# Optimization experiments

Hardware: AMD Instinct MI355X
Metric: run time of the kernel (lower is better)

The kernel has to match this reference:

```python
import jax, jax.numpy as jnp
import numpy as np

EMBEDDING_SIZE = 50
MAX_DOCUMENT_LENGTH = 100
MAX_LABEL = 15
VOCAB = 200000
HID = 1024
BATCH = 4096


def setup_inputs() -> dict:
    key = jax.random.key(0)
    ks = jax.random.split(key, 8)
    x = jax.random.randint(ks[0], (BATCH, MAX_DOCUMENT_LENGTH), 0, VOCAB)
    emb_table = jax.random.normal(ks[1], (VOCAB, EMBEDDING_SIZE), jnp.float32) * 0.05
    # Keras GRUCell (reset_after=True): kernel [E,3H], recurrent_kernel [H,3H],
    # bias [2,3H] split into input bias and recurrent bias; gate order z, r, h.
    kernel = jax.random.normal(ks[2], (EMBEDDING_SIZE, 3 * HID), jnp.float32) * (1.0 / np.sqrt(EMBEDDING_SIZE))
    rec_kernel = jax.random.normal(ks[3], (HID, 3 * HID), jnp.float32) * (1.0 / np.sqrt(HID))
    bias_i = jnp.zeros((3 * HID,), jnp.float32)
    bias_r = jnp.zeros((3 * HID,), jnp.float32)
    Wd = jax.random.normal(ks[4], (HID, MAX_LABEL), jnp.float32) * (1.0 / np.sqrt(HID))
    bd = jnp.zeros((MAX_LABEL,), jnp.float32)
    return {"x": x, "drop_rate": 0, "emb_table": emb_table, "kernel": kernel,
            "rec_kernel": rec_kernel, "bias_i": bias_i, "bias_r": bias_r,
            "Wd": Wd, "bd": bd}


def _gru_scan(emb, kernel, rec_kernel, bias_i, bias_r):
    # emb: [B,T,E] -> time-major [T,B,E]
    emb_t = jnp.transpose(emb, (1, 0, 2))
    B = emb.shape[0]
    h0 = jnp.zeros((B, HID), emb.dtype)

    def step(h, x_t):
        xp = x_t @ kernel + bias_i            # [B,3H]
        hp = h @ rec_kernel + bias_r          # [B,3H]
        xz, xr, xh = jnp.split(xp, 3, axis=-1)
        hz, hr, hh = jnp.split(hp, 3, axis=-1)
        z = jax.nn.sigmoid(xz + hz)
        r = jax.nn.sigmoid(xr + hr)
        hcand = jnp.tanh(xh + r * hh)
        h_new = z * h + (1.0 - z) * hcand
        return h_new, None

    h_last, _ = jax.lax.scan(step, h0, emb_t)
    return h_last


def reference(x, drop_rate, emb_table, kernel, rec_kernel, bias_i, bias_r, Wd, bd):
    emb = emb_table[x]                         # [B,T,E]
    encoding = _gru_scan(emb, kernel, rec_kernel, bias_i, bias_r)  # [B,H]
    if drop_rate > 0:                          # drop_rate is a static Python int
        keep = 1.0 - float(drop_rate)
        mask = jax.random.bernoulli(jax.random.key(1), keep, encoding.shape)
        encoding = jnp.where(mask, encoding / keep, 0.0)
    logits = encoding @ Wd + bd                # [B,15]
    return logits
```

## Files before the change

### kernel.cpp

```cpp
#include <hip/hip_runtime.h>
#include <stdint.h>

#define H_DIM   1024
#define G3      3072
#define EMB     50
#define TSTEPS  100
#define NB      4096
#define NLABEL  15

typedef __bf16 bf16x8 __attribute__((ext_vector_type(8)));
typedef float  f32x4  __attribute__((ext_vector_type(4)));

__device__ inline uint16_t f2bf(float f) {
  uint32_t u = __builtin_bit_cast(uint32_t, f);
  u += 0x7FFFu + ((u >> 16) & 1u);
  return (uint16_t)(u >> 16);
}

__device__ inline void gld16(const void* g, void* l) {
  __builtin_amdgcn_global_load_lds(
      (const __attribute__((address_space(1))) uint32_t*)g,
      (__attribute__((address_space(3))) uint32_t*)l, 16, 0, 0);
}

#define BARF() do { __builtin_amdgcn_s_barrier(); \
                    asm volatile("" ::: "memory"); } while (0)


__global__ __launch_bounds__(256) void prep_recT(const float* __restrict__ rec,
                                                 uint16_t* __restrict__ recT) {
  __shared__ uint16_t st[64][72];
  const int n0 = blockIdx.x * 64;
  const int k0 = blockIdx.y * 64;
  const int tid = threadIdx.x;
#pragma unroll
  for (int i = 0; i < 16; ++i) {
    int idx = tid + i * 256;
    int r = idx >> 6;
    int c = idx & 63;
    st[c][r] = f2bf(rec[(size_t)(k0 + r) * G3 + n0 + c]);
  }
  __syncthreads();
#pragma unroll
  for (int i = 0; i < 16; ++i) {
    int idx = tid + i * 256;
    int r = idx >> 6;
    int c = idx & 63;
    recT[(size_t)(n0 + r) * H_DIM + k0 + c] = st[r][c];
  }
}

__global__ __launch_bounds__(256) void prep_kerT(const float* __restrict__ ker,
                                                 uint16_t* __restrict__ kerT) {
  int n = blockIdx.x * 4 + (threadIdx.x >> 6);
  int k = threadIdx.x & 63;
  float v = (k < EMB) ? ker[(size_t)k * G3 + n] : 0.f;
  kerT[(size_t)n * 64 + k] = f2bf(v);
}

__global__ __launch_bounds__(256) void prep_embt(const int* __restrict__ x,
                                                 const float* __restrict__ tab,
                                                 uint16_t* __restrict__ embt) {
  int idx = blockIdx.x * 256 + threadIdx.x;
  int g = idx >> 5;
  int p = idx & 31;
  int t = g >> 12;
  int b = g & 4095;
  int row = x[b * TSTEPS + t];
  float2 v;
  if (p < 25) v = *reinterpret_cast<const float2*>(tab + (size_t)row * EMB + 2 * p);
  else { v.x = 0.f; v.y = 0.f; }
  uint32_t packed = (uint32_t)f2bf(v.x) | ((uint32_t)f2bf(v.y) << 16);
  *reinterpret_cast<uint32_t*>(embt + (size_t)g * 64 + 2 * p) = packed;
}

__global__ __launch_bounds__(512, 2) void gru_step_kernel(
    const uint16_t* __restrict__ hb_prev,
    float* __restrict__ hf,
    uint16_t* __restrict__ hb_next,
    const uint16_t* __restrict__ recT,
    const uint16_t* __restrict__ kerT,
    const uint16_t* __restrict__ embt,
    const float* __restrict__ bias_i,
    const float* __restrict__ bias_r) {
  __shared__ __align__(16) uint16_t sA2[2][128 * 64];
  __shared__ __align__(16) uint16_t sP[2][3][128 * 64];

  const int tid  = threadIdx.x;
  const int lane = tid & 63;
  const int wid  = tid >> 6;
  const int wm   = wid >> 2;
  const int wn   = wid & 3;
  const int bid  = blockIdx.x;
  const int xk = bid & 7, slot = bid >> 3;
  const int rowblk = (xk >> 1) * 8 + (slot >> 2);
  const int colblk = (xk & 1) * 4 + (slot & 3);
  const int r0 = rowblk * 128;
  const int j0 = colblk * 128;

  const int swz8 = 8 * ((lane & 7) ^ (lane >> 3));

  bf16x8 af[4][2];
  bf16x8 bf0[2][2], bf1[2][2];
  f32x4 accZ[4][2], accR[4][2], accH[4][2], accX[4][2];
#pragma unroll
  for (int m = 0; m < 4; ++m)
#pragma unroll
    for (int n = 0; n < 2; ++n) {
      accZ[m][n] = (f32x4){0.f, 0.f, 0.f, 0.f};
      accR[m][n] = (f32x4){0.f, 0.f, 0.f, 0.f};
      accH[m][n] = (f32x4){0.f, 0.f, 0.f, 0.f};
      accX[m][n] = (f32x4){0.f, 0.f, 0.f, 0.f};
    }

  auto stageA = [&](int t) {
    const int abuf = t & 1;
#pragma unroll
    for (int i = 0; i < 2; ++i) {
      int row = wid * 16 + i * 8 + (lane >> 3);
      const uint16_t* src = (t < 16)
          ? hb_prev + (size_t)(r0 + row) * H_DIM + t * 64 + swz8
          : embt + (size_t)(r0 + row) * 64 + swz8;
      gld16(src, &sA2[abuf][(wid * 128 + i * 64 + lane) * 8]);
    }
  };
  auto stageP = [&](int t, int g) {
    const int pbuf = t & 1;
#pragma unroll
    for (int i = 0; i < 2; ++i) {
      int c = wid * 2 + i;
      int n = c * 8 + (lane >> 3);
      const uint16_t* src = (t < 16)
          ? recT + ((size_t)g * H_DIM + j0 + n) * H_DIM + t * 64 + swz8
          : kerT + ((size_t)g * H_DIM + j0 + n) * 64 + swz8;
      gld16(src, &sP[pbuf][g][(c * 64 + lane) * 8]);
    }
  };
  auto readA = [&](int t) {
    const int abuf = t & 1;
#pragma unroll
    for (int ks = 0; ks < 2; ++ks) {
      const int colswz = (ks * 32 + (lane >> 4) * 8) ^ ((lane & 7) << 3);
#pragma unroll
      for (int mf = 0; mf < 4; ++mf)
        af[mf][ks] = *reinterpret_cast<const bf16x8*>(
            &sA2[abuf][(wm * 64 + mf * 16 + (lane & 15)) * 64 + colswz]);
    }
  };
  auto readB = [&](int t, int g, bf16x8 (&bf)[2][2]) {
    const int pbuf = t & 1;
#pragma unroll
    for (int ks = 0; ks < 2; ++ks) {
      const int colswz = (ks * 32 + (lane >> 4) * 8) ^ ((lane & 7) << 3);
#pragma unroll
      for (int nf = 0; nf < 2; ++nf) {
        int nn = wn * 32 + nf * 16 + (lane & 15);
        bf[nf][ks] = *reinterpret_cast<const bf16x8*>(&sP[pbuf][g][nn * 64 + colswz]);
      }
    }
  };
  auto MF = [&](bf16x8 (&bf)[2][2], f32x4 (&acc)[4][2]) {
    __builtin_amdgcn_s_setprio(1);
#pragma unroll
    for (int ks = 0; ks < 2; ++ks)
#pragma unroll
      for (int nf = 0; nf < 2; ++nf)
#pragma unroll
        for (int mf = 0; mf < 4; ++mf)
          acc[mf][nf] = __builtin_amdgcn_mfma_f32_16x16x32_bf16(
              af[mf][ks], bf[nf][ks], acc[mf][nf], 0, 0, 0);
    __builtin_amdgcn_s_setprio(0);
  };

#define PH(DSRD, MFBUF, MFACC, STG, WN) do { \
    DSRD; MF(MFBUF, MFACC); STG; \
    asm volatile("s_waitcnt vmcnt(" #WN ")" ::: "memory"); \
    BARF(); \
  } while (0)
#define PHH(MFBUF, MFACC, DSRD, STG, WN) do { \
    MF(MFBUF, MFACC); DSRD; STG; \
    asm volatile("s_waitcnt vmcnt(" #WN ")" ::: "memory"); \
    BARF(); \
  } while (0)
#define TILE_STEADY(t, BFA, BFB) do { \
    PH(readB(t, 1, BFB), BFA, accZ, stageP((t) + 1, 1), 6); \
    PH(readB(t, 2, BFA), BFB, accR, stageP((t) + 1, 2), 4); \
    PHH(BFA, accH, (readA((t) + 1), readB((t) + 1, 0, BFB)), \
        (stageA((t) + 2), stageP((t) + 2, 0)), 6); \
  } while (0)

  stageA(0); stageP(0, 0); stageP(0, 1); stageP(0, 2);
  stageA(1); stageP(1, 0);
  asm volatile("s_waitcnt vmcnt(0)" ::: "memory");
  BARF();
  readA(0); readB(0, 0, bf0);

  for (int tt = 0; tt < 14; tt += 2) {
    TILE_STEADY(tt, bf0, bf1);
    TILE_STEADY(tt + 1, bf1, bf0);
  }
  TILE_STEADY(14, bf0, bf1);
  PH(readB(15, 1, bf0), bf1, accZ, stageP(16, 1), 6);
  PH(readB(15, 2, bf1), bf0, accR, stageP(16, 2), 4);
  PHH(bf1, accH, (readA(16), readB(16, 0, bf0)), (void)0, 2);
  PH(readB(16, 1, bf1), bf0, accZ, (void)0, 0);
  PH(readB(16, 2, bf0), bf1, accR, (void)0, 0);
  MF(bf0, accX);

#pragma unroll
  for (int nf = 0; nf < 2; ++nf) {
    int col = j0 + wn * 32 + nf * 16 + (lane & 15);
    float b_z = bias_i[col] + bias_r[col];
    float b_r = bias_i[H_DIM + col] + bias_r[H_DIM + col];
    float bih = bias_i[2 * H_DIM + col];
    float brh = bias_r[2 * H_DIM + col];
#pragma unroll
    for (int mf = 0; mf < 4; ++mf) {
#pragma unroll
      for (int q = 0; q < 4; ++q) {
        int row = r0 + wm * 64 + mf * 16 + (lane >> 4) * 4 + q;
        float z  = 1.f / (1.f + __expf(-(accZ[mf][nf][q] + b_z)));
        float rr = 1.f / (1.f + __expf(-(accR[mf][nf][q] + b_r)));
        float pre = accX[mf][nf][q] + bih + rr * (accH[mf][nf][q] + brh);
        float hc  = 2.f / (1.f + __expf(-2.f * pre)) - 1.f;
        size_t idx = (size_t)row * H_DIM + col;
        float hold = hf[idx];
        float hnew = z * hold + (1.f - z) * hc;
        hf[idx] = hnew;
        hb_next[idx] = f2bf(hnew);
      }
    }
  }
#undef PH
#undef PHH
#undef TILE_STEADY
}

__global__ __launch_bounds__(64) void logits_kernel(const float* __restrict__ hf,
                                                    const float* __restrict__ Wd,
                                                    const float* __restrict__ bd,
                                                    float* __restrict__ out) {
  int b = blockIdx.x;
  int l = threadIdx.x;
  float p[NLABEL];
#pragma unroll
  for (int o = 0; o < NLABEL; ++o) p[o] = 0.f;
  for (int kb = 0; kb < 16; ++kb) {
    int k = kb * 64 + l;
    float hv = hf[(size_t)b * H_DIM + k];
#pragma unroll
    for (int o = 0; o < NLABEL; ++o) p[o] += hv * Wd[k * NLABEL + o];
  }
#pragma unroll
  for (int o = 0; o < NLABEL; ++o) {
#pragma unroll
    for (int s = 32; s; s >>= 1) p[o] += __shfl_xor(p[o], s);
  }
  if (l == 0) {
#pragma unroll
    for (int o = 0; o < NLABEL; ++o) out[(size_t)b * NLABEL + o] = p[o] + bd[o];
  }
}

extern "C" void kernel_launch(void* const* d_in, const int* in_sizes, int n_in,
                              void* d_out, int out_size, void* d_ws, size_t ws_size,
                              hipStream_t stream) {
  const int*   x          = (const int*)d_in[0];
  const float* emb_table  = (const float*)d_in[2];
  const float* kernel_w   = (const float*)d_in[3];
  const float* rec_kernel = (const float*)d_in[4];
  const float* bias_i     = (const float*)d_in[5];
  const float* bias_r     = (const float*)d_in[6];
  const float* Wd         = (const float*)d_in[7];
  const float* bd         = (const float*)d_in[8];
  float* out = (float*)d_out;

  char* ws = (char*)d_ws;
  size_t off = 0;
  auto alloc = [&](size_t bytes) {
    char* p = ws + off;
    off += (bytes + 255) & ~(size_t)255;
    return p;
  };
  float*    hf   = (float*)alloc((size_t)NB * H_DIM * 4);
  uint16_t* hb0  = (uint16_t*)alloc((size_t)NB * H_DIM * 2);
  uint16_t* hb1  = (uint16_t*)alloc((size_t)NB * H_DIM * 2);
  uint16_t* recT = (uint16_t*)alloc((size_t)G3 * H_DIM * 2);
  uint16_t* kerT = (uint16_t*)alloc((size_t)G3 * 64 * 2);
  uint16_t* embt = (uint16_t*)alloc((size_t)TSTEPS * NB * 64 * 2);
  if (off > ws_size) return;

  hipMemsetAsync(hf, 0, (size_t)NB * H_DIM * 4, stream);
  hipMemsetAsync(hb0, 0, (size_t)NB * H_DIM * 2, stream);

  prep_recT<<<dim3(G3 / 64, H_DIM / 64), 256, 0, stream>>>(rec_kernel, recT);
  prep_kerT<<<G3 / 4, 256, 0, stream>>>(kernel_w, kerT);
  prep_embt<<<TSTEPS * NB * 32 / 256, 256, 0, stream>>>(x, emb_table, embt);

  uint16_t* hb[2] = {hb0, hb1};
  for (int t = 0; t < TSTEPS; ++t) {
    gru_step_kernel<<<256, 512, 0, stream>>>(
        hb[t & 1], hf, hb[(t + 1) & 1], recT, kerT,
        embt + (size_t)t * NB * 64, bias_i, bias_r);
  }
  logits_kernel<<<NB, 64, 0, stream>>>(hf, Wd, bd, out);
}
```

Before: 3.458 ms.

## Fuse GRU timesteps into one persistent cooperative kernel with per-rowblock barriers

Replaces the 100 per-timestep kernel launches with a single cooperative persistent kernel that loops over timesteps. The fp32 hidden state stays in registers instead of being read and written in global memory each step, and hf is written only at the final step. Blocks sharing a row block synchronise through an atomic counter. This is meant to remove launch gaps and global h traffic. It relies on all 256 blocks being co-resident and adds spin-wait barrier overhead.

```diff
diff --git a/kernel.cpp b/kernel.cpp
--- a/kernel.cpp
+++ b/kernel.cpp
@@ -74,15 +74,16 @@
   *reinterpret_cast<uint32_t*>(embt + (size_t)g * 64 + 2 * p) = packed;
 }
 
-__global__ __launch_bounds__(512, 2) void gru_step_kernel(
-    const uint16_t* __restrict__ hb_prev,
+__global__ __launch_bounds__(512, 2) void gru_persistent(
+    uint16_t* __restrict__ hb0,
+    uint16_t* __restrict__ hb1,
     float* __restrict__ hf,
-    uint16_t* __restrict__ hb_next,
     const uint16_t* __restrict__ recT,
     const uint16_t* __restrict__ kerT,
-    const uint16_t* __restrict__ embt,
+    const uint16_t* __restrict__ embt_all,
     const float* __restrict__ bias_i,
-    const float* __restrict__ bias_r) {
+    const float* __restrict__ bias_r,
+    uint32_t* __restrict__ cnt) {
   __shared__ __align__(16) uint16_t sA2[2][128 * 64];
   __shared__ __align__(16) uint16_t sP[2][3][128 * 64];
 
@@ -100,77 +101,99 @@
 
   const int swz8 = 8 * ((lane & 7) ^ (lane >> 3));
 
+  float c_bz[2], c_br[2], c_bih[2], c_brh[2];
+#pragma unroll
+  for (int nf = 0; nf < 2; ++nf) {
+    int col = j0 + wn * 32 + nf * 16 + (lane & 15);
+    c_bz[nf]  = bias_i[col] + bias_r[col];
+    c_br[nf]  = bias_i[H_DIM + col] + bias_r[H_DIM + col];
+    c_bih[nf] = bias_i[2 * H_DIM + col];
+    c_brh[nf] = bias_r[2 * H_DIM + col];
+  }
+
+  f32x4 hreg[4][2];
+#pragma unroll
+  for (int m = 0; m < 4; ++m)
+#pragma unroll
+    for (int n = 0; n < 2; ++n) hreg[m][n] = (f32x4){0.f, 0.f, 0.f, 0.f};
+
   bf16x8 af[4][2];
   bf16x8 bf0[2][2], bf1[2][2];
   f32x4 accZ[4][2], accR[4][2], accH[4][2], accX[4][2];
-#pragma unroll
-  for (int m = 0; m < 4; ++m)
-#pragma unroll
-    for (int n = 0; n < 2; ++n) {
-      accZ[m][n] = (f32x4){0.f, 0.f, 0.f, 0.f};
-      accR[m][n] = (f32x4){0.f, 0.f, 0.f, 0.f};
-      accH[m][n] = (f32x4){0.f, 0.f, 0.f, 0.f};
-      accX[m][n] = (f32x4){0.f, 0.f, 0.f, 0.f};
-    }
-
-  auto stageA = [&](int t) {
-    const int abuf = t & 1;
-#pragma unroll
-    for (int i = 0; i < 2; ++i) {
-      int row = wid * 16 + i * 8 + (lane >> 3);
-      const uint16_t* src = (t < 16)
-          ? hb_prev + (size_t)(r0 + row) * H_DIM + t * 64 + swz8
-          : embt + (size_t)(r0 + row) * 64 + swz8;
-      gld16(src, &sA2[abuf][(wid * 128 + i * 64 + lane) * 8]);
-    }
-  };
-  auto stageP = [&](int t, int g) {
-    const int pbuf = t & 1;
-#pragma unroll
-    for (int i = 0; i < 2; ++i) {
-      int c = wid * 2 + i;
-      int n = c * 8 + (lane >> 3);
-      const uint16_t* src = (t < 16)
-          ? recT + ((size_t)g * H_DIM + j0 + n) * H_DIM + t * 64 + swz8
-          : kerT + ((size_t)g * H_DIM + j0 + n) * 64 + swz8;
-      gld16(src, &sP[pbuf][g][(c * 64 + lane) * 8]);
-    }
-  };
-  auto readA = [&](int t) {
-    const int abuf = t & 1;
-#pragma unroll
-    for (int ks = 0; ks < 2; ++ks) {
-      const int colswz = (ks * 32 + (lane >> 4) * 8) ^ ((lane & 7) << 3);
-#pragma unroll
-      for (int mf = 0; mf < 4; ++mf)
-        af[mf][ks] = *reinterpret_cast<const bf16x8*>(
-            &sA2[abuf][(wm * 64 + mf * 16 + (lane & 15)) * 64 + colswz]);
-    }
-  };
-  auto readB = [&](int t, int g, bf16x8 (&bf)[2][2]) {
-    const int pbuf = t & 1;
-#pragma unroll
-    for (int ks = 0; ks < 2; ++ks) {
-      const int colswz = (ks * 32 + (lane >> 4) * 8) ^ ((lane & 7) << 3);
-#pragma unroll
-      for (int nf = 0; nf < 2; ++nf) {
-        int nn = wn * 32 + nf * 16 + (lane & 15);
-        bf[nf][ks] = *reinterpret_cast<const bf16x8*>(&sP[pbuf][g][nn * 64 + colswz]);
-      }
-    }
-  };
-  auto MF = [&](bf16x8 (&bf)[2][2], f32x4 (&acc)[4][2]) {
-    __builtin_amdgcn_s_setprio(1);
-#pragma unroll
-    for (int ks = 0; ks < 2; ++ks)
-#pragma unroll
-      for (int nf = 0; nf < 2; ++nf)
+
+  for (int s = 0; s < TSTEPS; ++s) {
+    const uint16_t* __restrict__ hb_prev = (s & 1) ? hb1 : hb0;
+    uint16_t* __restrict__ hb_next       = (s & 1) ? hb0 : hb1;
+    const uint16_t* __restrict__ emb = embt_all + (size_t)s * NB * 64;
+
+#pragma unroll
+    for (int m = 0; m < 4; ++m)
+#pragma unroll
+      for (int n = 0; n < 2; ++n) {
+        accZ[m][n] = (f32x4){0.f, 0.f, 0.f, 0.f};
+        accR[m][n] = (f32x4){0.f, 0.f, 0.f, 0.f};
+        accH[m][n] = (f32x4){0.f, 0.f, 0.f, 0.f};
+        accX[m][n] = (f32x4){0.f, 0.f, 0.f, 0.f};
+      }
+
+    auto stageA = [&](int t) {
+      const int abuf = t & 1;
+#pragma unroll
+      for (int i = 0; i < 2; ++i) {
+        int row = wid * 16 + i * 8 + (lane >> 3);
+        const uint16_t* src = (t < 16)
+            ? hb_prev + (size_t)(r0 + row) * H_DIM + t * 64 + swz8
+            : emb + (size_t)(r0 + row) * 64 + swz8;
+        gld16(src, &sA2[abuf][(wid * 128 + i * 64 + lane) * 8]);
+      }
+    };
+    auto stageP = [&](int t, int g) {
+      const int pbuf = t & 1;
+#pragma unroll
+      for (int i = 0; i < 2; ++i) {
+        int c = wid * 2 + i;
+        int n = c * 8 + (lane >> 3);
+        const uint16_t* src = (t < 16)
+            ? recT + ((size_t)g * H_DIM + j0 + n) * H_DIM + t * 64 + swz8
+            : kerT + ((size_t)g * H_DIM + j0 + n) * 64 + swz8;
+        gld16(src, &sP[pbuf][g][(c * 64 + lane) * 8]);
+      }
+    };
+    auto readA = [&](int t) {
+      const int abuf = t & 1;
+#pragma unroll
+      for (int ks = 0; ks < 2; ++ks) {
+        const int colswz = (ks * 32 + (lane >> 4) * 8) ^ ((lane & 7) << 3);
 #pragma unroll
         for (int mf = 0; mf < 4; ++mf)
-          acc[mf][nf] = __builtin_amdgcn_mfma_f32_16x16x32_bf16(
-              af[mf][ks], bf[nf][ks], acc[mf][nf], 0, 0, 0);
-    __builtin_amdgcn_s_setprio(0);
-  };
+          af[mf][ks] = *reinterpret_cast<const bf16x8*>(
+              &sA2[abuf][(wm * 64 + mf * 16 + (lane & 15)) * 64 + colswz]);
+      }
+    };
+    auto readB = [&](int t, int g, bf16x8 (&bf)[2][2]) {
+      const int pbuf = t & 1;
+#pragma unroll
+      for (int ks = 0; ks < 2; ++ks) {
+        const int colswz = (ks * 32 + (lane >> 4) * 8) ^ ((lane & 7) << 3);
+#pragma unroll
+        for (int nf = 0; nf < 2; ++nf) {
+          int nn = wn * 32 + nf * 16 + (lane & 15);
+          bf[nf][ks] = *reinterpret_cast<const bf16x8*>(&sP[pbuf][g][nn * 64 + colswz]);
+        }
+      }
+    };
+    auto MF = [&](bf16x8 (&bf)[2][2], f32x4 (&acc)[4][2]) {
+      __builtin_amdgcn_s_setprio(1);
+#pragma unroll
+      for (int ks = 0; ks < 2; ++ks)
+#pragma unroll
+        for (int nf = 0; nf < 2; ++nf)
+#pragma unroll
+          for (int mf = 0; mf < 4; ++mf)
+            acc[mf][nf] = __builtin_amdgcn_mfma_f32_16x16x32_bf16(
+                af[mf][ks], bf[nf][ks], acc[mf][nf], 0, 0, 0);
+      __builtin_amdgcn_s_setprio(0);
+    };
 
 #define PH(DSRD, MFBUF, MFACC, STG, WN) do { \
     DSRD; MF(MFBUF, MFACC); STG; \
@@ -189,51 +212,62 @@
         (stageA((t) + 2), stageP((t) + 2, 0)), 6); \
   } while (0)
 
-  stageA(0); stageP(0, 0); stageP(0, 1); stageP(0, 2);
-  stageA(1); stageP(1, 0);
-  asm volatile("s_waitcnt vmcnt(0)" ::: "memory");
-  BARF();
-  readA(0); readB(0, 0, bf0);
-
-  for (int tt = 0; tt < 14; tt += 2) {
-    TILE_STEADY(tt, bf0, bf1);
-    TILE_STEADY(tt + 1, bf1, bf0);
-  }
-  TILE_STEADY(14, bf0, bf1);
-  PH(readB(15, 1, bf0), bf1, accZ, stageP(16, 1), 6);
-  PH(readB(15, 2, bf1), bf0, accR, stageP(16, 2), 4);
-  PHH(bf1, accH, (readA(16), readB(16, 0, bf0)), (void)0, 2);
-  PH(readB(16, 1, bf1), bf0, accZ, (void)0, 0);
-  PH(readB(16, 2, bf0), bf1, accR, (void)0, 0);
-  MF(bf0, accX);
-
-#pragma unroll
-  for (int nf = 0; nf < 2; ++nf) {
-    int col = j0 + wn * 32 + nf * 16 + (lane & 15);
-    float b_z = bias_i[col] + bias_r[col];
-    float b_r = bias_i[H_DIM + col] + bias_r[H_DIM + col];
-    float bih = bias_i[2 * H_DIM + col];
-    float brh = bias_r[2 * H_DIM + col];
-#pragma unroll
-    for (int mf = 0; mf < 4; ++mf) {
-#pragma unroll
-      for (int q = 0; q < 4; ++q) {
-        int row = r0 + wm * 64 + mf * 16 + (lane >> 4) * 4 + q;
-        float z  = 1.f / (1.f + __expf(-(accZ[mf][nf][q] + b_z)));
-        float rr = 1.f / (1.f + __expf(-(accR[mf][nf][q] + b_r)));
-        float pre = accX[mf][nf][q] + bih + rr * (accH[mf][nf][q] + brh);
-        float hc  = 2.f / (1.f + __expf(-2.f * pre)) - 1.f;
-        size_t idx = (size_t)row * H_DIM + col;
-        float hold = hf[idx];
-        float hnew = z * hold + (1.f - z) * hc;
-        hf[idx] = hnew;
-        hb_next[idx] = f2bf(hnew);
-      }
+    stageA(0); stageP(0, 0); stageP(0, 1); stageP(0, 2);
+    stageA(1); stageP(1, 0);
+    asm volatile("s_waitcnt vmcnt(0)" ::: "memory");
+    BARF();
+    readA(0); readB(0, 0, bf0);
+
+    for (int tt = 0; tt < 14; tt += 2) {
+      TILE_STEADY(tt, bf0, bf1);
+      TILE_STEADY(tt + 1, bf1, bf0);
     }
-  }
+    TILE_STEADY(14, bf0, bf1);
+    PH(readB(15, 1, bf0), bf1, accZ, stageP(16, 1), 6);
+    PH(readB(15, 2, bf1), bf0, accR, stageP(16, 2), 4);
+    PHH(bf1, accH, (readA(16), readB(16, 0, bf0)), (void)0, 2);
+    PH(readB(16, 1, bf1), bf0, accZ, (void)0, 0);
+    PH(readB(16, 2, bf0), bf1, accR, (void)0, 0);
+    MF(bf0, accX);
+
 #undef PH
 #undef PHH
 #undef TILE_STEADY
+
+#pragma unroll
+    for (int nf = 0; nf < 2; ++nf) {
+      int col = j0 + wn * 32 + nf * 16 + (lane & 15);
+#pragma unroll
+      for (int mf = 0; mf < 4; ++mf) {
+#pragma unroll
+        for (int q = 0; q < 4; ++q) {
+          int row = r0 + wm * 64 + mf * 16 + (lane >> 4) * 4 + q;
+          float z  = 1.f / (1.f + __expf(-(accZ[mf][nf][q] + c_bz[nf])));
+          float rr = 1.f / (1.f + __expf(-(accR[mf][nf][q] + c_br[nf])));
+          float pre = accX[mf][nf][q] + c_bih[nf] +
+                      rr * (accH[mf][nf][q] + c_brh[nf]);
+          float hc  = 2.f / (1.f + __expf(-2.f * pre)) - 1.f;
+          float hnew = z * hreg[mf][nf][q] + (1.f - z) * hc;
+          hreg[mf][nf][q] = hnew;
+          size_t idx = (size_t)row * H_DIM + col;
+          hb_next[idx] = f2bf(hnew);
+          if (s == TSTEPS - 1) hf[idx] = hnew;
+        }
+      }
+    }
+
+    __syncthreads();
+    if (tid == 0) {
+      __threadfence();
+      __hip_atomic_fetch_add(&cnt[rowblk], 1u, __ATOMIC_RELEASE,
+                             __HIP_MEMORY_SCOPE_AGENT);
+      const uint32_t target = 8u * (uint32_t)(s + 1);
+      while (__hip_atomic_load(&cnt[rowblk], __ATOMIC_ACQUIRE,
+                               __HIP_MEMORY_SCOPE_AGENT) < target)
+        __builtin_amdgcn_s_sleep(2);
+    }
+    __syncthreads();
+  }
 }
 
 __global__ __launch_bounds__(64) void logits_kernel(const float* __restrict__ hf,
@@ -288,20 +322,24 @@
   uint16_t* recT = (uint16_t*)alloc((size_t)G3 * H_DIM * 2);
   uint16_t* kerT = (uint16_t*)alloc((size_t)G3 * 64 * 2);
   uint16_t* embt = (uint16_t*)alloc((size_t)TSTEPS * NB * 64 * 2);
+  uint32_t* cnt  = (uint32_t*)alloc(256);
   if (off > ws_size) return;
 
-  hipMemsetAsync(hf, 0, (size_t)NB * H_DIM * 4, stream);
   hipMemsetAsync(hb0, 0, (size_t)NB * H_DIM * 2, stream);
+  hipMemsetAsync(cnt, 0, 256, stream);
 
   prep_recT<<<dim3(G3 / 64, H_DIM / 64), 256, 0, stream>>>(rec_kernel, recT);
   prep_kerT<<<G3 / 4, 256, 0, stream>>>(kernel_w, kerT);
   prep_embt<<<TSTEPS * NB * 32 / 256, 256, 0, stream>>>(x, emb_table, embt);
 
-  uint16_t* hb[2] = {hb0, hb1};
-  for (int t = 0; t < TSTEPS; ++t) {
-    gru_step_kernel<<<256, 512, 0, stream>>>(
-        hb[t & 1], hf, hb[(t + 1) & 1], recT, kerT,
-        embt + (size_t)t * NB * 64, bias_i, bias_r);
-  }
+  const uint16_t* embt_c = embt;
+  const uint16_t* recT_c = recT;
+  const uint16_t* kerT_c = kerT;
+  void* kargs[] = {(void*)&hb0, (void*)&hb1, (void*)&hf,
+                   (void*)&recT_c, (void*)&kerT_c, (void*)&embt_c,
+                   (void*)&bias_i, (void*)&bias_r, (void*)&cnt};
+  hipLaunchCooperativeKernel(reinterpret_cast<void*>(gru_persistent),
+                             dim3(256), dim3(512), kargs, 0, stream);
+
   logits_kernel<<<NB, 64, 0, stream>>>(hf, Wd, bd, out);
 }
```

After: 6.225 ms. 80.0% more time.
